# Optimization experiments

Measured on AMD Instinct MI355X. Metric: run time of the kernel, lower is better.

Reference implementation:

```python
import jax, jax.numpy as jnp
import numpy as np

B, T, F_FEAT = 2048, 128, 8
UO, UI = 128, 64
BN_EPS = 1e-3  # keras BatchNormalization default epsilon


def _lstm(x, Wk, Wr, b):
    """Keras-style LSTM, activation=selu, recurrent_activation=sigmoid.
    x: [B,T,Fin]; Wk: [Fin,4U] (gate order i,f,c,o); Wr: [U,4U]; b: [4U].
    Returns full hidden sequence [B,T,U]. Inference mode (no dropout)."""
    U = Wr.shape[0]
    xz = jnp.einsum('btf,fg->btg', x, Wk) + b        # precompute input projections
    xz = jnp.swapaxes(xz, 0, 1)                      # [T,B,4U]

    def step(carry, zx):
        h, c = carry
        z = zx + h @ Wr                              # [B,4U]
        i, f, g, o = jnp.split(z, 4, axis=-1)
        i = jax.nn.sigmoid(i)
        f = jax.nn.sigmoid(f)
        g = jax.nn.selu(g)
        o = jax.nn.sigmoid(o)
        c = f * c + i * g
        h = o * jax.nn.selu(c)
        return (h, c), h

    h0 = jnp.zeros((x.shape[0], U), x.dtype)
    (_, _), hs = jax.lax.scan(step, (h0, jnp.zeros_like(h0)), xz)
    return jnp.swapaxes(hs, 0, 1)                    # [B,T,U]


def _bn(x, gamma, beta, mean, var):
    # inference-mode BatchNormalization over last (channel) axis
    return (x - mean) * (gamma / jnp.sqrt(var + BN_EPS)) + beta


def setup_inputs() -> dict:
    key = jax.random.key(0)
    ks = jax.random.split(key, 40)
    w = lambda k, shape, s=0.08: jax.random.normal(k, shape, jnp.float32) * s
    inp = {}
    inp['x'] = jax.random.normal(ks[0], (B, T, F_FEAT), jnp.float32)
    # encoder outer LSTM + BN
    inp['Wk1'] = w(ks[1], (F_FEAT, 4 * UO)); inp['Wr1'] = w(ks[2], (UO, 4 * UO)); inp['b1'] = jnp.zeros((4 * UO,), jnp.float32)
    inp['g1'] = 1.0 + w(ks[3], (UO,)); inp['be1'] = w(ks[4], (UO,)); inp['m1'] = w(ks[5], (UO,)); inp['v1'] = 0.5 + jax.random.uniform(ks[6], (UO,), jnp.float32)
    # encoder inner LSTM + BN
    inp['Wk2'] = w(ks[7], (UO, 4 * UI)); inp['Wr2'] = w(ks[8], (UI, 4 * UI)); inp['b2'] = jnp.zeros((4 * UI,), jnp.float32)
    inp['g2'] = 1.0 + w(ks[9], (UI,)); inp['be2'] = w(ks[10], (UI,)); inp['m2'] = w(ks[11], (UI,)); inp['v2'] = 0.5 + jax.random.uniform(ks[12], (UI,), jnp.float32)
    # decoder inner LSTM + BN
    inp['Wk3'] = w(ks[13], (UI, 4 * UI)); inp['Wr3'] = w(ks[14], (UI, 4 * UI)); inp['b3'] = jnp.zeros((4 * UI,), jnp.float32)
    inp['g3'] = 1.0 + w(ks[15], (UI,)); inp['be3'] = w(ks[16], (UI,)); inp['m3'] = w(ks[17], (UI,)); inp['v3'] = 0.5 + jax.random.uniform(ks[18], (UI,), jnp.float32)
    # decoder outer LSTM + BN
    inp['Wk4'] = w(ks[19], (UI, 4 * UO)); inp['Wr4'] = w(ks[20], (UO, 4 * UO)); inp['b4'] = jnp.zeros((4 * UO,), jnp.float32)
    inp['g4'] = 1.0 + w(ks[21], (UO,)); inp['be4'] = w(ks[22], (UO,)); inp['m4'] = w(ks[23], (UO,)); inp['v4'] = 0.5 + jax.random.uniform(ks[24], (UO,), jnp.float32)
    # per-feature TimeDistributed Dense(1) heads fused into one [UO,F] matmul
    inp['Wd'] = w(ks[25], (UO, F_FEAT)); inp['bd'] = jnp.zeros((F_FEAT,), jnp.float32)
    return inp


def reference(x, Wk1, Wr1, b1, g1, be1, m1, v1,
              Wk2, Wr2, b2, g2, be2, m2, v2,
              Wk3, Wr3, b3, g3, be3, m3, v3,
              Wk4, Wr4, b4, g4, be4, m4, v4,
              Wd, bd):
    # encoder
    h = _bn(_lstm(x, Wk1, Wr1, b1), g1, be1, m1, v1)          # [B,T,UO]
    enc = _lstm(h, Wk2, Wr2, b2)[:, -1]                        # return_sequences=False
    enc = _bn(enc, g2, be2, m2, v2)                            # [B,UI]
    # decoder: RepeatVector(T)
    d = jnp.broadcast_to(enc[:, None, :], (enc.shape[0], T, enc.shape[1]))
    d = _bn(_lstm(d, Wk3, Wr3, b3), g3, be3, m3, v3)           # [B,T,UI]
    d = _bn(_lstm(d, Wk4, Wr4, b4), g4, be4, m4, v4)           # [B,T,UO]
    out = jnp.einsum('btu,uf->btf', d, Wd) + bd                # per-feature Dense(1) heads
    return out                                                 # [B,T,F] (== stacked decoded features)
```

## Files before the change

kernel.cpp:

```cpp
#include <hip/hip_runtime.h>
#include <math.h>


typedef _Float16 half8 __attribute__((ext_vector_type(8)));
typedef __attribute__((ext_vector_type(4))) float floatx4;

#define TT 128
#define NF 8
#define BT 8
#define NBLK 256
#define NTH 512

#define FS_Z1 0
#define FS_Z2 160
#define FS_X3 256
#define FS_Z3 288
#define FS_Z4 320
#define FS_DN 512
#define FS_EXT 516
#define N_FRAGS 516

#define MFMAH(a,b,c) __builtin_amdgcn_mfma_f32_16x16x32_f16((a),(b),(c),0,0,0)
#define PINA(v) asm volatile("" : "+a"(v))

__device__ __forceinline__ float sigmoid_(float x){
    return __builtin_amdgcn_rcpf(1.0f + __expf(-x));
}
__device__ __forceinline__ float selu_(float x){
    const float alpha = 1.6732632423543772f, scale = 1.0507009873554805f;
    return x > 0.0f ? scale*x : scale*alpha*(__expf(x)-1.0f);
}

__global__ void pack_kernel(const float* __restrict__ Wk1, const float* __restrict__ Wr1,
                            const float* __restrict__ Wk2, const float* __restrict__ Wr2,
                            const float* __restrict__ Wk3, const float* __restrict__ Wr3,
                            const float* __restrict__ Wk4, const float* __restrict__ Wr4,
                            const float* __restrict__ Wd,
                            const float* __restrict__ g3, const float* __restrict__ v3,
                            const float* __restrict__ g4, const float* __restrict__ v4,
                            unsigned short* __restrict__ ws)
{
    const int g = blockIdx.x;
    const int l = threadIdx.x;
    int blob, fs, KS;
    if      (g < FS_Z2){ blob = 0; fs = FS_Z1; KS = 5; }
    else if (g < FS_X3){ blob = 1; fs = FS_Z2; KS = 6; }
    else if (g < FS_Z3){ blob = 2; fs = FS_X3; KS = 2; }
    else if (g < FS_Z4){ blob = 3; fs = FS_Z3; KS = 2; }
    else if (g < FS_DN){ blob = 4; fs = FS_Z4; KS = 6; }
    else               { blob = 5; fs = FS_DN; KS = 4; }
    const int fl = g - fs;
    const int tile = fl / KS, kk = fl % KS;
    const int c   = l & 15;
    const int col = tile * 16 + c;
    const int k0  = kk * 32 + (l >> 4) * 8;
    const int oc2 = (2*(tile&1) + (c>>3))*64 + 8*(tile>>1) + (c&7);

    half8 v8;
    #pragma unroll
    for (int j = 0; j < 8; ++j){
        const int k = k0 + j;
        float v = 0.0f;
        switch (blob){
            case 0: v = (k < 128) ? Wr1[k*512 + col] : (k < 136 ? Wk1[(k-128)*512 + col] : 0.0f); break;
            case 1: v = (k < 128) ? Wk2[k*256 + oc2] : Wr2[(k-128)*256 + oc2]; break;
            case 2: v = Wk3[k*256 + oc2]; break;
            case 3: v = Wr3[k*256 + oc2]; break;
            case 4: v = (k < 64) ? Wk4[k*512 + col] * (g3[k]*rsqrtf(v3[k]+1e-3f))
                                 : Wr4[(k-64)*512 + col]; break;
            case 5: v = (col < 8) ? Wd[k*8 + col] * (g4[k]*rsqrtf(v4[k]+1e-3f)) : 0.0f; break;
        }
        v8[j] = (_Float16)v;
    }
    *(half8*)(ws + (size_t)g*512 + l*8) = v8;
}

__global__ void foldbias_kernel(const float* __restrict__ b4, const float* __restrict__ bd,
                                const float* __restrict__ g3, const float* __restrict__ be3,
                                const float* __restrict__ m3, const float* __restrict__ v3,
                                const float* __restrict__ g4, const float* __restrict__ be4,
                                const float* __restrict__ m4, const float* __restrict__ v4,
                                const float* __restrict__ Wk4, const float* __restrict__ Wd,
                                unsigned short* __restrict__ ws)
{
    float* wsf = (float*)(ws + (size_t)FS_EXT*512);
    const int tid = threadIdx.x;
    float s = b4[tid];
    for (int k = 0; k < 64; ++k){
        float s3 = g3[k]*rsqrtf(v3[k]+1e-3f);
        float t3 = be3[k] - m3[k]*s3;
        s += t3 * Wk4[k*512 + tid];
    }
    wsf[tid] = s;
    if (tid < 8){
        float d = bd[tid];
        for (int k = 0; k < 128; ++k){
            float s4 = g4[k]*rsqrtf(v4[k]+1e-3f);
            float t4 = be4[k] - m4[k]*s4;
            d += t4 * Wd[k*8 + tid];
        }
        wsf[512 + tid] = d;
    }
}

__global__ __launch_bounds__(NTH, 1) void lstm_ae_mfma(
    const float* __restrict__ x,
    const float* __restrict__ b1, const float* __restrict__ b2,
    const float* __restrict__ b3, const float* __restrict__ b4,
    const float* __restrict__ bd,
    const float* __restrict__ g1, const float* __restrict__ be1, const float* __restrict__ m1, const float* __restrict__ v1,
    const float* __restrict__ g2, const float* __restrict__ be2, const float* __restrict__ m2, const float* __restrict__ v2,
    const float* __restrict__ g3, const float* __restrict__ be3, const float* __restrict__ m3, const float* __restrict__ v3,
    const float* __restrict__ g4, const float* __restrict__ be4, const float* __restrict__ m4, const float* __restrict__ v4,
    const unsigned short* __restrict__ WS,
    float* __restrict__ out)
{
    __shared__ __align__(16) _Float16 AZ1[2][5][512];
    __shared__ __align__(16) _Float16 AH1B[2][4][512];
    __shared__ __align__(16) _Float16 AH2[2][2][512];
    __shared__ __align__(16) _Float16 AH3[2][2][512];
    __shared__ __align__(16) _Float16 AH4[2][4][512];
    __shared__ __align__(16) _Float16 ENC[2][512];

    const int tid = threadIdx.x;
    const int w = tid >> 6, l = tid & 63;
    const int l15 = l & 15, q = l >> 4;
    const int h8 = (l15 >> 3) & 1;
    const int b0 = blockIdx.x * BT;
    const int arow0 = 4*q;

    const int u1 = 16*w + l15;
    const int kk1 = u1 >> 5;
    const int sbase1 = ((u1>>3)&3)*128 + (u1&7);
    const float s1v = g1[u1]*rsqrtf(v1[u1]+1e-3f), t1v = be1[u1]-m1[u1]*s1v;

    const int un = 8*w + (l15 & 7);
    const int s2w = (w&3)*128 + (arow0 + h8)*8 + (l15&7);
    const float s2v = g2[un]*rsqrtf(v2[un]+1e-3f), t2v = be2[un]-m2[un]*s2v;

    const float* wsf = (const float*)(WS + (size_t)FS_EXT*512);

    float z1b[4], z4b[4], z2b[2], z3b[2];
    #pragma unroll
    for (int i = 0; i < 4; ++i){
        z1b[i] = b1[(w + 8*i)*16 + l15];
        z4b[i] = wsf[(w + 8*i)*16 + l15];
    }
    #pragma unroll
    for (int i = 0; i < 2; ++i){
        z2b[i] = b2[(2*i + h8)*64 + un];
        z3b[i] = b3[(2*i + h8)*64 + un];
    }
    const float bdv = (w == 4 && l15 < 8) ? wsf[512 + l15] : 0.0f;

    half8 wz1[4][5], wz2[2][6];
    #pragma unroll
    for (int i = 0; i < 4; ++i)
        #pragma unroll
        for (int kk = 0; kk < 5; ++kk){
            wz1[i][kk] = *(const half8*)(WS + (size_t)(FS_Z1 + (w+8*i)*5 + kk)*512 + l*8);
            PINA(wz1[i][kk]);
        }
    #pragma unroll
    for (int i = 0; i < 2; ++i)
        #pragma unroll
        for (int kk = 0; kk < 6; ++kk){
            wz2[i][kk] = *(const half8*)(WS + (size_t)(FS_Z2 + (2*w+i)*6 + kk)*512 + l*8);
            PINA(wz2[i][kk]);
        }

    for (int i = tid; i < 2560; i += NTH) ((int*)AZ1)[i] = 0;
    for (int i = tid; i < 2048; i += NTH){ ((int*)AH1B)[i] = 0; ((int*)AH4)[i] = 0; }
    for (int i = tid; i < 1024; i += NTH){ ((int*)AH2)[i] = 0; ((int*)AH3)[i] = 0; }
    for (int i = tid; i < 512;  i += NTH) ((int*)ENC)[i] = 0;
    if (tid < 64){
        const int br = tid >> 3, ar = (br & 1) + 4*(br >> 1);
        AZ1[0][4][ar*8 + (tid&7)] = (_Float16)x[(size_t)(b0+br)*(TT*NF) + (tid&7)];
    }
    float c1r[2] = {0,0}, c4r[2] = {0,0};
    float c2r = 0.0f, c3r = 0.0f, h2last = 0.0f;
    __syncthreads();

    for (int t = -1; t < TT; ++t){
        const int pe = t & 1;
        if (t + 1 < TT){
            float xnext = 0.0f;
            if (tid < 64 && t + 2 < TT)
                xnext = x[(size_t)(b0+(tid>>3))*(TT*NF) + (size_t)(t+2)*NF + (tid&7)];

            floatx4 acc[4];
            #pragma unroll
            for (int i = 0; i < 4; ++i) acc[i] = (floatx4){z1b[i],z1b[i],z1b[i],z1b[i]};
            #pragma unroll
            for (int kk = 0; kk < 5; ++kk){
                half8 a = *(const half8*)&AZ1[pe^1][kk][l*8];
                #pragma unroll
                for (int i = 0; i < 4; ++i)
                    acc[i] = MFMAH(a, wz1[i][kk], acc[i]);
            }
            #pragma unroll
            for (int r = 0; r < 2; ++r){
                float ig = sigmoid_(acc[0][r]);
                float fg = sigmoid_(acc[1][r]);
                float gg = selu_(acc[2][r]);
                float og = sigmoid_(acc[3][r]);
                float c = fg*c1r[r] + ig*gg; c1r[r] = c;
                float h = og*selu_(c);
                const int s = sbase1 + (arow0 + r)*8;
                AZ1[pe][kk1][s]    = (_Float16)h;
                AH1B[pe^1][kk1][s] = (_Float16)(h*s1v + t1v);
            }
            if (tid < 64 && t + 2 < TT){
                const int br = tid >> 3, ar = (br & 1) + 4*(br >> 1);
                AZ1[pe][4][ar*8 + (tid&7)] = (_Float16)xnext;
            }
        }
        if (t >= 0){
            floatx4 a2[2];
            #pragma unroll
            for (int i = 0; i < 2; ++i) a2[i] = (floatx4){z2b[i],z2b[i],z2b[i],z2b[i]};
            #pragma unroll
            for (int kk = 0; kk < 6; ++kk){
                half8 a = (kk < 4) ? *(const half8*)&AH1B[pe][kk][l*8]
                                   : *(const half8*)&AH2[pe][kk-4][l*8];
                #pragma unroll
                for (int i = 0; i < 2; ++i)
                    a2[i] = MFMAH(a, wz2[i][kk], a2[i]);
            }
            float keep0 = h8 ? a2[0][1] : a2[0][0];
            float keep1 = h8 ? a2[1][1] : a2[1][0];
            float give0 = h8 ? a2[0][0] : a2[0][1];
            float give1 = h8 ? a2[1][0] : a2[1][1];
            float e0 = __shfl_xor(give0, 8);
            float e1 = __shfl_xor(give1, 8);
            float zi = h8 ? e0    : keep0;
            float zf = h8 ? keep0 : e0;
            float zg = h8 ? e1    : keep1;
            float zo = h8 ? keep1 : e1;
            float ig = sigmoid_(zi);
            float fg = sigmoid_(zf);
            float gg = selu_(zg);
            float og = sigmoid_(zo);
            float c = fg*c2r + ig*gg; c2r = c;
            h2last = og*selu_(c);
            AH2[pe^1][w>>2][s2w] = (_Float16)h2last;
        }
        __syncthreads();
    }

    ENC[w>>2][s2w] = (_Float16)(h2last*s2v + t2v);
    __syncthreads();
    floatx4 xz3r[2];
    #pragma unroll
    for (int i = 0; i < 2; ++i) xz3r[i] = (floatx4){z3b[i],z3b[i],z3b[i],z3b[i]};
    #pragma unroll
    for (int kk = 0; kk < 2; ++kk){
        half8 a = *(const half8*)&ENC[kk][l*8];
        #pragma unroll
        for (int i = 0; i < 2; ++i){
            half8 b = *(const half8*)(WS + (size_t)(FS_X3 + (2*w+i)*2 + kk)*512 + l*8);
            xz3r[i] = MFMAH(a, b, xz3r[i]);
        }
    }

    half8 wz4[4][6], wr3[2][2], wd4[4];
    #pragma unroll
    for (int i = 0; i < 4; ++i)
        #pragma unroll
        for (int kk = 0; kk < 6; ++kk){
            wz4[i][kk] = *(const half8*)(WS + (size_t)(FS_Z4 + (w+8*i)*6 + kk)*512 + l*8);
            PINA(wz4[i][kk]);
        }
    #pragma unroll
    for (int i = 0; i < 2; ++i)
        #pragma unroll
        for (int kk = 0; kk < 2; ++kk){
            wr3[i][kk] = *(const half8*)(WS + (size_t)(FS_Z3 + (2*w+i)*2 + kk)*512 + l*8);
            PINA(wr3[i][kk]);
        }
    if (w == 4){
        #pragma unroll
        for (int kk = 0; kk < 4; ++kk){
            wd4[kk] = *(const half8*)(WS + (size_t)(FS_DN + kk)*512 + l*8);
            PINA(wd4[kk]);
        }
    }
    __syncthreads();

    for (int t = -1; t < TT; ++t){
        const int pd = t & 1;
        half8 a3k0 = *(const half8*)&AH3[pd^1][0][l*8];
        half8 a3k1 = *(const half8*)&AH3[pd^1][1][l*8];
        if (t + 1 < TT){
            floatx4 a3[2];
            a3[0] = xz3r[0]; a3[1] = xz3r[1];
            #pragma unroll
            for (int i = 0; i < 2; ++i){
                a3[i] = MFMAH(a3k0, wr3[i][0], a3[i]);
                a3[i] = MFMAH(a3k1, wr3[i][1], a3[i]);
            }
            float keep0 = h8 ? a3[0][1] : a3[0][0];
            float keep1 = h8 ? a3[1][1] : a3[1][0];
            float give0 = h8 ? a3[0][0] : a3[0][1];
            float give1 = h8 ? a3[1][0] : a3[1][1];
            float e0 = __shfl_xor(give0, 8);
            float e1 = __shfl_xor(give1, 8);
            float zi = h8 ? e0    : keep0;
            float zf = h8 ? keep0 : e0;
            float zg = h8 ? e1    : keep1;
            float zo = h8 ? keep1 : e1;
            float ig = sigmoid_(zi);
            float fg = sigmoid_(zf);
            float gg = selu_(zg);
            float og = sigmoid_(zo);
            float c = fg*c3r + ig*gg; c3r = c;
            float h = og*selu_(c);
            AH3[pd][w>>2][s2w] = (_Float16)h;
        }
        if (w == 4 && t > 0){
            floatx4 ad = (floatx4){bdv,bdv,bdv,bdv};
            #pragma unroll
            for (int kk = 0; kk < 4; ++kk){
                half8 a = *(const half8*)&AH4[pd][kk][l*8];
                ad = MFMAH(a, wd4[kk], ad);
            }
            if (l15 < 8){
                #pragma unroll
                for (int r = 0; r < 2; ++r)
                    out[(size_t)(b0 + 2*q + r)*(TT*NF) + (size_t)(t-1)*NF + l15] = ad[r];
            }
        }
        if (t >= 0){
            floatx4 a4[4];
            #pragma unroll
            for (int i = 0; i < 4; ++i) a4[i] = (floatx4){z4b[i],z4b[i],z4b[i],z4b[i]};
            #pragma unroll
            for (int i = 0; i < 4; ++i){
                a4[i] = MFMAH(a3k0, wz4[i][0], a4[i]);
                a4[i] = MFMAH(a3k1, wz4[i][1], a4[i]);
            }
            #pragma unroll
            for (int kk = 2; kk < 6; ++kk){
                half8 a = *(const half8*)&AH4[pd][kk-2][l*8];
                #pragma unroll
                for (int i = 0; i < 4; ++i)
                    a4[i] = MFMAH(a, wz4[i][kk], a4[i]);
            }
            #pragma unroll
            for (int r = 0; r < 2; ++r){
                float ig = sigmoid_(a4[0][r]);
                float fg = sigmoid_(a4[1][r]);
                float gg = selu_(a4[2][r]);
                float og = sigmoid_(a4[3][r]);
                float c = fg*c4r[r] + ig*gg; c4r[r] = c;
                float h = og*selu_(c);
                const int s = sbase1 + (arow0 + r)*8;
                AH4[pd^1][kk1][s] = (_Float16)h;
            }
        }
        __syncthreads();
    }

    if (w == 4){
        floatx4 ad = (floatx4){bdv,bdv,bdv,bdv};
        #pragma unroll
        for (int kk = 0; kk < 4; ++kk){
            half8 a = *(const half8*)&AH4[0][kk][l*8];
            ad = MFMAH(a, wd4[kk], ad);
        }
        if (l15 < 8){
            #pragma unroll
            for (int r = 0; r < 2; ++r)
                out[(size_t)(b0 + 2*q + r)*(TT*NF) + (size_t)(TT-1)*NF + l15] = ad[r];
        }
    }
}

extern "C" void kernel_launch(void* const* d_in, const int* in_sizes, int n_in,
                              void* d_out, int out_size, void* d_ws, size_t ws_size,
                              hipStream_t stream) {
    const float* x   = (const float*)d_in[0];
    const float* Wk1 = (const float*)d_in[1];  const float* Wr1 = (const float*)d_in[2];
    const float* b1  = (const float*)d_in[3];
    const float* g1  = (const float*)d_in[4];  const float* be1 = (const float*)d_in[5];
    const float* m1  = (const float*)d_in[6];  const float* v1  = (const float*)d_in[7];
    const float* Wk2 = (const float*)d_in[8];  const float* Wr2 = (const float*)d_in[9];
    const float* b2  = (const float*)d_in[10];
    const float* g2  = (const float*)d_in[11]; const float* be2 = (const float*)d_in[12];
    const float* m2  = (const float*)d_in[13]; const float* v2  = (const float*)d_in[14];
    const float* Wk3 = (const float*)d_in[15]; const float* Wr3 = (const float*)d_in[16];
    const float* b3  = (const float*)d_in[17];
    const float* g3  = (const float*)d_in[18]; const float* be3 = (const float*)d_in[19];
    const float* m3  = (const float*)d_in[20]; const float* v3  = (const float*)d_in[21];
    const float* Wk4 = (const float*)d_in[22]; const float* Wr4 = (const float*)d_in[23];
    const float* b4  = (const float*)d_in[24];
    const float* g4  = (const float*)d_in[25]; const float* be4 = (const float*)d_in[26];
    const float* m4  = (const float*)d_in[27]; const float* v4  = (const float*)d_in[28];
    const float* Wd  = (const float*)d_in[29]; const float* bd  = (const float*)d_in[30];

    unsigned short* ws = (unsigned short*)d_ws;

    pack_kernel<<<dim3(N_FRAGS), dim3(64), 0, stream>>>(Wk1, Wr1, Wk2, Wr2, Wk3, Wr3,
                                                        Wk4, Wr4, Wd, g3, v3, g4, v4, ws);
    foldbias_kernel<<<dim3(1), dim3(512), 0, stream>>>(b4, bd, g3, be3, m3, v3,
                                                       g4, be4, m4, v4, Wk4, Wd, ws);
    lstm_ae_mfma<<<dim3(NBLK), dim3(NTH), 0, stream>>>(
        x, b1, b2, b3, b4, bd,
        g1, be1, m1, v1, g2, be2, m2, v2,
        g3, be3, m3, v3, g4, be4, m4, v4,
        (const unsigned short*)ws, (float*)d_out);
}
```

Baseline: 445.0 us.

## Fold BN1/BN2 into packed weights and prescale gates by log2e

Batch-norm scales for layers 1 and 2 are folded into the Wk2/Wk3 fragments, and their shifts into precomputed biases. This lets layer 2 reuse the raw layer-1 hidden fragments already loaded for layer 1, removing the separate AH1B and ENC shared buffers and their per-step writes. All gate weights and biases are also prescaled by log2(e) so sigmoid and the selu gate use a native exp2 without a multiply. The risk is extra fp16 rounding from folding scales into half-precision weights, plus a slightly larger prologue in the fold kernel.

```diff
diff --git a/kernel.cpp b/kernel.cpp
--- a/kernel.cpp
+++ b/kernel.cpp
@@ -20,11 +20,23 @@
 #define FS_EXT 516
 #define N_FRAGS 516
 
+#define LOG2E 1.4426950408889634f
+
 #define MFMAH(a,b,c) __builtin_amdgcn_mfma_f32_16x16x32_f16((a),(b),(c),0,0,0)
 #define PINA(v) asm volatile("" : "+a"(v))
 
-__device__ __forceinline__ float sigmoid_(float x){
-    return __builtin_amdgcn_rcpf(1.0f + __expf(-x));
+__device__ __forceinline__ float exp2_(float x){
+#if __has_builtin(__builtin_amdgcn_exp2f)
+    return __builtin_amdgcn_exp2f(x);
+#else
+    return __expf(x * 0.6931471805599453f);
+#endif
+}
+__device__ __forceinline__ float sigmoid2_(float x){
+    return __builtin_amdgcn_rcpf(1.0f + exp2_(-x));
+}
+__device__ __forceinline__ float selug2_(float x){
+    return x > 0.0f ? 0.7282904281f*x : 1.7580993408473766f*(exp2_(x)-1.0f);
 }
 __device__ __forceinline__ float selu_(float x){
     const float alpha = 1.6732632423543772f, scale = 1.0507009873554805f;
@@ -36,6 +48,8 @@
                             const float* __restrict__ Wk3, const float* __restrict__ Wr3,
                             const float* __restrict__ Wk4, const float* __restrict__ Wr4,
                             const float* __restrict__ Wd,
+                            const float* __restrict__ g1, const float* __restrict__ v1,
+                            const float* __restrict__ g2, const float* __restrict__ v2,
                             const float* __restrict__ g3, const float* __restrict__ v3,
                             const float* __restrict__ g4, const float* __restrict__ v4,
                             unsigned short* __restrict__ ws)
@@ -62,12 +76,13 @@
         const int k = k0 + j;
         float v = 0.0f;
         switch (blob){
-            case 0: v = (k < 128) ? Wr1[k*512 + col] : (k < 136 ? Wk1[(k-128)*512 + col] : 0.0f); break;
-            case 1: v = (k < 128) ? Wk2[k*256 + oc2] : Wr2[(k-128)*256 + oc2]; break;
-            case 2: v = Wk3[k*256 + oc2]; break;
-            case 3: v = Wr3[k*256 + oc2]; break;
-            case 4: v = (k < 64) ? Wk4[k*512 + col] * (g3[k]*rsqrtf(v3[k]+1e-3f))
-                                 : Wr4[(k-64)*512 + col]; break;
+            case 0: v = ((k < 128) ? Wr1[k*512 + col] : (k < 136 ? Wk1[(k-128)*512 + col] : 0.0f)) * LOG2E; break;
+            case 1: v = ((k < 128) ? Wk2[k*256 + oc2] * (g1[k]*rsqrtf(v1[k]+1e-3f))
+                                   : Wr2[(k-128)*256 + oc2]) * LOG2E; break;
+            case 2: v = Wk3[k*256 + oc2] * (g2[k]*rsqrtf(v2[k]+1e-3f)) * LOG2E; break;
+            case 3: v = Wr3[k*256 + oc2] * LOG2E; break;
+            case 4: v = ((k < 64) ? Wk4[k*512 + col] * (g3[k]*rsqrtf(v3[k]+1e-3f))
+                                  : Wr4[(k-64)*512 + col]) * LOG2E; break;
             case 5: v = (col < 8) ? Wd[k*8 + col] * (g4[k]*rsqrtf(v4[k]+1e-3f)) : 0.0f; break;
         }
         v8[j] = (_Float16)v;
@@ -75,52 +90,64 @@
     *(half8*)(ws + (size_t)g*512 + l*8) = v8;
 }
 
-__global__ void foldbias_kernel(const float* __restrict__ b4, const float* __restrict__ bd,
+__global__ void foldbias_kernel(const float* __restrict__ b2, const float* __restrict__ b3,
+                                const float* __restrict__ b4, const float* __restrict__ bd,
+                                const float* __restrict__ g1, const float* __restrict__ be1,
+                                const float* __restrict__ m1, const float* __restrict__ v1,
+                                const float* __restrict__ g2, const float* __restrict__ be2,
+                                const float* __restrict__ m2, const float* __restrict__ v2,
                                 const float* __restrict__ g3, const float* __restrict__ be3,
                                 const float* __restrict__ m3, const float* __restrict__ v3,
                                 const float* __restrict__ g4, const float* __restrict__ be4,
                                 const float* __restrict__ m4, const float* __restrict__ v4,
+                                const float* __restrict__ Wk2, const float* __restrict__ Wk3,
                                 const float* __restrict__ Wk4, const float* __restrict__ Wd,
                                 unsigned short* __restrict__ ws)
 {
     float* wsf = (float*)(ws + (size_t)FS_EXT*512);
     const int tid = threadIdx.x;
-    float s = b4[tid];
-    for (int k = 0; k < 64; ++k){
-        float s3 = g3[k]*rsqrtf(v3[k]+1e-3f);
-        float t3 = be3[k] - m3[k]*s3;
-        s += t3 * Wk4[k*512 + tid];
-    }
-    wsf[tid] = s;
+    {
+        float s = b4[tid];
+        for (int k = 0; k < 64; ++k){
+            float s3 = g3[k]*rsqrtf(v3[k]+1e-3f);
+            s += (be3[k] - m3[k]*s3) * Wk4[k*512 + tid];
+        }
+        wsf[tid] = s * LOG2E;
+    }
     if (tid < 8){
         float d = bd[tid];
         for (int k = 0; k < 128; ++k){
             float s4 = g4[k]*rsqrtf(v4[k]+1e-3f);
-            float t4 = be4[k] - m4[k]*s4;
-            d += t4 * Wd[k*8 + tid];
+            d += (be4[k] - m4[k]*s4) * Wd[k*8 + tid];
         }
         wsf[512 + tid] = d;
+    }
+    if (tid < 256){
+        float s = b2[tid];
+        for (int k = 0; k < 128; ++k){
+            float s1 = g1[k]*rsqrtf(v1[k]+1e-3f);
+            s += (be1[k] - m1[k]*s1) * Wk2[k*256 + tid];
+        }
+        wsf[520 + tid] = s * LOG2E;
+        float u = b3[tid];
+        for (int k = 0; k < 64; ++k){
+            float s2 = g2[k]*rsqrtf(v2[k]+1e-3f);
+            u += (be2[k] - m2[k]*s2) * Wk3[k*256 + tid];
+        }
+        wsf[776 + tid] = u * LOG2E;
     }
 }
 
 __global__ __launch_bounds__(NTH, 1) void lstm_ae_mfma(
     const float* __restrict__ x,
-    const float* __restrict__ b1, const float* __restrict__ b2,
-    const float* __restrict__ b3, const float* __restrict__ b4,
-    const float* __restrict__ bd,
-    const float* __restrict__ g1, const float* __restrict__ be1, const float* __restrict__ m1, const float* __restrict__ v1,
-    const float* __restrict__ g2, const float* __restrict__ be2, const float* __restrict__ m2, const float* __restrict__ v2,
-    const float* __restrict__ g3, const float* __restrict__ be3, const float* __restrict__ m3, const float* __restrict__ v3,
-    const float* __restrict__ g4, const float* __restrict__ be4, const float* __restrict__ m4, const float* __restrict__ v4,
+    const float* __restrict__ b1,
     const unsigned short* __restrict__ WS,
     float* __restrict__ out)
 {
     __shared__ __align__(16) _Float16 AZ1[2][5][512];
-    __shared__ __align__(16) _Float16 AH1B[2][4][512];
     __shared__ __align__(16) _Float16 AH2[2][2][512];
     __shared__ __align__(16) _Float16 AH3[2][2][512];
     __shared__ __align__(16) _Float16 AH4[2][4][512];
-    __shared__ __align__(16) _Float16 ENC[2][512];
 
     const int tid = threadIdx.x;
     const int w = tid >> 6, l = tid & 63;
@@ -132,24 +159,22 @@
     const int u1 = 16*w + l15;
     const int kk1 = u1 >> 5;
     const int sbase1 = ((u1>>3)&3)*128 + (u1&7);
-    const float s1v = g1[u1]*rsqrtf(v1[u1]+1e-3f), t1v = be1[u1]-m1[u1]*s1v;
 
     const int un = 8*w + (l15 & 7);
     const int s2w = (w&3)*128 + (arow0 + h8)*8 + (l15&7);
-    const float s2v = g2[un]*rsqrtf(v2[un]+1e-3f), t2v = be2[un]-m2[un]*s2v;
 
     const float* wsf = (const float*)(WS + (size_t)FS_EXT*512);
 
     float z1b[4], z4b[4], z2b[2], z3b[2];
     #pragma unroll
     for (int i = 0; i < 4; ++i){
-        z1b[i] = b1[(w + 8*i)*16 + l15];
+        z1b[i] = b1[(w + 8*i)*16 + l15] * LOG2E;
         z4b[i] = wsf[(w + 8*i)*16 + l15];
     }
     #pragma unroll
     for (int i = 0; i < 2; ++i){
-        z2b[i] = b2[(2*i + h8)*64 + un];
-        z3b[i] = b3[(2*i + h8)*64 + un];
+        z2b[i] = wsf[520 + (2*i + h8)*64 + un];
+        z3b[i] = wsf[776 + (2*i + h8)*64 + un];
     }
     const float bdv = (w == 4 && l15 < 8) ? wsf[512 + l15] : 0.0f;
 
@@ -170,19 +195,22 @@
         }
 
     for (int i = tid; i < 2560; i += NTH) ((int*)AZ1)[i] = 0;
-    for (int i = tid; i < 2048; i += NTH){ ((int*)AH1B)[i] = 0; ((int*)AH4)[i] = 0; }
+    for (int i = tid; i < 2048; i += NTH) ((int*)AH4)[i] = 0;
     for (int i = tid; i < 1024; i += NTH){ ((int*)AH2)[i] = 0; ((int*)AH3)[i] = 0; }
-    for (int i = tid; i < 512;  i += NTH) ((int*)ENC)[i] = 0;
     if (tid < 64){
         const int br = tid >> 3, ar = (br & 1) + 4*(br >> 1);
         AZ1[0][4][ar*8 + (tid&7)] = (_Float16)x[(size_t)(b0+br)*(TT*NF) + (tid&7)];
     }
     float c1r[2] = {0,0}, c4r[2] = {0,0};
-    float c2r = 0.0f, c3r = 0.0f, h2last = 0.0f;
+    float c2r = 0.0f, c3r = 0.0f;
     __syncthreads();
 
     for (int t = -1; t < TT; ++t){
         const int pe = t & 1;
+        half8 a5[5];
+        #pragma unroll
+        for (int kk = 0; kk < 5; ++kk)
+            a5[kk] = *(const half8*)&AZ1[pe^1][kk][l*8];
         if (t + 1 < TT){
             float xnext = 0.0f;
             if (tid < 64 && t + 2 < TT)
@@ -192,23 +220,19 @@
             #pragma unroll
             for (int i = 0; i < 4; ++i) acc[i] = (floatx4){z1b[i],z1b[i],z1b[i],z1b[i]};
             #pragma unroll
-            for (int kk = 0; kk < 5; ++kk){
-                half8 a = *(const half8*)&AZ1[pe^1][kk][l*8];
+            for (int kk = 0; kk < 5; ++kk)
                 #pragma unroll
                 for (int i = 0; i < 4; ++i)
-                    acc[i] = MFMAH(a, wz1[i][kk], acc[i]);
-            }
+                    acc[i] = MFMAH(a5[kk], wz1[i][kk], acc[i]);
             #pragma unroll
             for (int r = 0; r < 2; ++r){
-                float ig = sigmoid_(acc[0][r]);
-                float fg = sigmoid_(acc[1][r]);
-                float gg = selu_(acc[2][r]);
-                float og = sigmoid_(acc[3][r]);
+                float ig = sigmoid2_(acc[0][r]);
+                float fg = sigmoid2_(acc[1][r]);
+                float gg = selug2_(acc[2][r]);
+                float og = sigmoid2_(acc[3][r]);
                 float c = fg*c1r[r] + ig*gg; c1r[r] = c;
                 float h = og*selu_(c);
-                const int s = sbase1 + (arow0 + r)*8;
-                AZ1[pe][kk1][s]    = (_Float16)h;
-                AH1B[pe^1][kk1][s] = (_Float16)(h*s1v + t1v);
+                AZ1[pe][kk1][sbase1 + (arow0 + r)*8] = (_Float16)h;
             }
             if (tid < 64 && t + 2 < TT){
                 const int br = tid >> 3, ar = (br & 1) + 4*(br >> 1);
@@ -220,9 +244,13 @@
             #pragma unroll
             for (int i = 0; i < 2; ++i) a2[i] = (floatx4){z2b[i],z2b[i],z2b[i],z2b[i]};
             #pragma unroll
-            for (int kk = 0; kk < 6; ++kk){
-                half8 a = (kk < 4) ? *(const half8*)&AH1B[pe][kk][l*8]
-                                   : *(const half8*)&AH2[pe][kk-4][l*8];
+            for (int kk = 0; kk < 4; ++kk)
+                #pragma unroll
+                for (int i = 0; i < 2; ++i)
+                    a2[i] = MFMAH(a5[kk], wz2[i][kk], a2[i]);
+            #pragma unroll
+            for (int kk = 4; kk < 6; ++kk){
+                half8 a = *(const half8*)&AH2[pe][kk-4][l*8];
                 #pragma unroll
                 for (int i = 0; i < 2; ++i)
                     a2[i] = MFMAH(a, wz2[i][kk], a2[i]);
@@ -237,25 +265,23 @@
             float zf = h8 ? keep0 : e0;
             float zg = h8 ? e1    : keep1;
             float zo = h8 ? keep1 : e1;
-            float ig = sigmoid_(zi);
-            float fg = sigmoid_(zf);
-            float gg = selu_(zg);
-            float og = sigmoid_(zo);
+            float ig = sigmoid2_(zi);
+            float fg = sigmoid2_(zf);
+            float gg = selug2_(zg);
+            float og = sigmoid2_(zo);
             float c = fg*c2r + ig*gg; c2r = c;
-            h2last = og*selu_(c);
-            AH2[pe^1][w>>2][s2w] = (_Float16)h2last;
+            float h2 = og*selu_(c);
+            AH2[pe^1][w>>2][s2w] = (_Float16)h2;
         }
         __syncthreads();
     }
 
-    ENC[w>>2][s2w] = (_Float16)(h2last*s2v + t2v);
-    __syncthreads();
     floatx4 xz3r[2];
     #pragma unroll
     for (int i = 0; i < 2; ++i) xz3r[i] = (floatx4){z3b[i],z3b[i],z3b[i],z3b[i]};
     #pragma unroll
     for (int kk = 0; kk < 2; ++kk){
-        half8 a = *(const half8*)&ENC[kk][l*8];
+        half8 a = *(const half8*)&AH2[0][kk][l*8];
         #pragma unroll
         for (int i = 0; i < 2; ++i){
             half8 b = *(const half8*)(WS + (size_t)(FS_X3 + (2*w+i)*2 + kk)*512 + l*8);
@@ -309,10 +335,10 @@
             float zf = h8 ? keep0 : e0;
             float zg = h8 ? e1    : keep1;
             float zo = h8 ? keep1 : e1;
-            float ig = sigmoid_(zi);
-            float fg = sigmoid_(zf);
-            float gg = selu_(zg);
-            float og = sigmoid_(zo);
+            float ig = sigmoid2_(zi);
+            float fg = sigmoid2_(zf);
+            float gg = selug2_(zg);
+            float og = sigmoid2_(zo);
             float c = fg*c3r + ig*gg; c3r = c;
             float h = og*selu_(c);
             AH3[pd][w>>2][s2w] = (_Float16)h;
@@ -348,14 +374,13 @@
             }
             #pragma unroll
             for (int r = 0; r < 2; ++r){
-                float ig = sigmoid_(a4[0][r]);
-                float fg = sigmoid_(a4[1][r]);
-                float gg = selu_(a4[2][r]);
-                float og = sigmoid_(a4[3][r]);
+                float ig = sigmoid2_(a4[0][r]);
+                float fg = sigmoid2_(a4[1][r]);
+                float gg = selug2_(a4[2][r]);
+                float og = sigmoid2_(a4[3][r]);
                 float c = fg*c4r[r] + ig*gg; c4r[r] = c;
                 float h = og*selu_(c);
-                const int s = sbase1 + (arow0 + r)*8;
-                AH4[pd^1][kk1][s] = (_Float16)h;
+                AH4[pd^1][kk1][sbase1 + (arow0 + r)*8] = (_Float16)h;
             }
         }
         __syncthreads();
@@ -401,12 +426,12 @@
     unsigned short* ws = (unsigned short*)d_ws;
 
     pack_kernel<<<dim3(N_FRAGS), dim3(64), 0, stream>>>(Wk1, Wr1, Wk2, Wr2, Wk3, Wr3,
-                                                        Wk4, Wr4, Wd, g3, v3, g4, v4, ws);
-    foldbias_kernel<<<dim3(1), dim3(512), 0, stream>>>(b4, bd, g3, be3, m3, v3,
-                                                       g4, be4, m4, v4, Wk4, Wd, ws);
+                                                        Wk4, Wr4, Wd,
+                                                        g1, v1, g2, v2, g3, v3, g4, v4, ws);
+    foldbias_kernel<<<dim3(1), dim3(512), 0, stream>>>(b2, b3, b4, bd,
+                                                       g1, be1, m1, v1, g2, be2, m2, v2,
+                                                       g3, be3, m3, v3, g4, be4, m4, v4,
+                                                       Wk2, Wk3, Wk4, Wd, ws);
     lstm_ae_mfma<<<dim3(NBLK), dim3(NTH), 0, stream>>>(
-        x, b1, b2, b3, b4, bd,
-        g1, be1, m1, v1, g2, be2, m2, v2,
-        g3, be3, m3, v3, g4, be4, m4, v4,
-        (const unsigned short*)ws, (float*)d_out);
-}
+        x, b1, (const unsigned short*)ws, (float*)d_out);
+}
```

New measurement: 436.7 us. About the same (-1.9%).
